# Kernel optimization log

Hardware: AMD Instinct MI355X
Metric: run time of the kernel (lower is better)

Reference implementation:

```python
import jax, jax.numpy as jnp
import numpy as np

B = 8
T, H, W = 8, 56, 56
C = 128
NH = 4
HD = C // NH
WS = (2, 7, 7)
SS = (1, 3, 3)
N = WS[0] * WS[1] * WS[2]  # 98 tokens per window
HID = 4 * C
SCALE = HD ** -0.5
RPB_SIZE = (2 * WS[0] - 1) * (2 * WS[1] - 1) * (2 * WS[2] - 1)  # 507
EPS = 1e-5


def _rel_index():
    # [N, N] int index into relative position bias table
    coords = np.stack(np.meshgrid(np.arange(WS[0]), np.arange(WS[1]), np.arange(WS[2]), indexing='ij'))
    cf = coords.reshape(3, -1)
    rel = (cf[:, :, None] - cf[:, None, :]).transpose(1, 2, 0)
    rel[:, :, 0] += WS[0] - 1
    rel[:, :, 1] += WS[1] - 1
    rel[:, :, 2] += WS[2] - 1
    rel[:, :, 0] *= (2 * WS[1] - 1) * (2 * WS[2] - 1)
    rel[:, :, 1] *= 2 * WS[2] - 1
    return rel.sum(-1)


def _np_window_partition_mask(img):
    # img: [1,T,H,W,1] -> [nW, N]
    m = img.reshape(1, T // WS[0], WS[0], H // WS[1], WS[1], W // WS[2], WS[2], 1)
    m = m.transpose(0, 1, 3, 5, 2, 4, 6, 7).reshape(-1, N)
    return m


def _attn_mask():
    # standard shifted-window mask: [nW, N, N] with 0 / -100
    img = np.zeros((1, T, H, W, 1), np.float32)
    cnt = 0
    slices = lambda w, s: (slice(0, -w), slice(-w, -s), slice(-s, None))
    for t in slices(WS[0], SS[0]):
        for h in slices(WS[1], SS[1]):
            for w in slices(WS[2], SS[2]):
                img[:, t, h, w, :] = cnt
                cnt += 1
    mw = _np_window_partition_mask(img)
    am = mw[:, None, :] - mw[:, :, None]
    return np.where(am != 0, np.float32(-100.0), np.float32(0.0))


REL_IDX = jnp.asarray(_rel_index())          # [N, N]
ATTN_MASK = jnp.asarray(_attn_mask())        # [nW, N, N]


def window_partition(x):
    # x: [B,T,H,W,C] -> [B*nW, N, C]
    x = x.reshape(B, T // WS[0], WS[0], H // WS[1], WS[1], W // WS[2], WS[2], C)
    return x.transpose(0, 1, 3, 5, 2, 4, 6, 7).reshape(-1, N, C)


def window_reverse(w):
    # w: [B*nW, N, C] -> [B,T,H,W,C]
    x = w.reshape(B, T // WS[0], H // WS[1], W // WS[2], WS[0], WS[1], WS[2], C)
    return x.transpose(0, 1, 4, 2, 5, 3, 6, 7).reshape(B, T, H, W, C)


def layernorm(x, g, b):
    mu = x.mean(-1, keepdims=True)
    var = ((x - mu) ** 2).mean(-1, keepdims=True)
    return (x - mu) * jax.lax.rsqrt(var + EPS) * g + b


def setup_inputs() -> dict:
    key = jax.random.key(0)
    ks = jax.random.split(key, 8)
    p = lambda k, shp: jax.random.normal(k, shp, jnp.float32) * 0.02
    return {
        'x': jax.random.normal(ks[0], (B, T * H * W, C), jnp.float32),
        'norm1_g': jnp.ones((C,), jnp.float32), 'norm1_b': jnp.zeros((C,), jnp.float32),
        'qkv_w': p(ks[1], (C, 3 * C)), 'qkv_b': jnp.zeros((3 * C,), jnp.float32),
        'proj_w': p(ks[2], (C, C)), 'proj_b': jnp.zeros((C,), jnp.float32),
        'rpb_table': p(ks[3], (RPB_SIZE, NH)),
        'norm2_g': jnp.ones((C,), jnp.float32), 'norm2_b': jnp.zeros((C,), jnp.float32),
        'fc1_w': p(ks[4], (C, HID)), 'fc1_b': jnp.zeros((HID,), jnp.float32),
        'fc2_w': p(ks[5], (HID, C)), 'fc2_b': jnp.zeros((C,), jnp.float32),
    }


def reference(x, norm1_g, norm1_b, qkv_w, qkv_b, proj_w, proj_b, rpb_table,
              norm2_g, norm2_b, fc1_w, fc1_b, fc2_w, fc2_b):
    shortcut = x
    h = layernorm(x, norm1_g, norm1_b).reshape(B, T, H, W, C)
    # cyclic shift
    h = jnp.roll(h, (-SS[0], -SS[1], -SS[2]), axis=(1, 2, 3))
    xw = window_partition(h)                                   # [B_, N, C]
    B_ = xw.shape[0]
    qkv = (xw @ qkv_w + qkv_b).reshape(B_, N, 3, NH, HD)
    qkv = qkv.transpose(2, 0, 3, 1, 4)                         # [3, B_, NH, N, HD]
    q, k, v = qkv[0] * SCALE, qkv[1], qkv[2]
    attn = jnp.einsum('bhnd,bhmd->bhnm', q, k)                 # [B_, NH, N, N]
    bias = rpb_table[REL_IDX.reshape(-1)].reshape(N, N, NH).transpose(2, 0, 1)
    attn = attn + bias[None]
    nW = ATTN_MASK.shape[0]
    attn = attn.reshape(B_ // nW, nW, NH, N, N) + ATTN_MASK[None, :, None]
    attn = jax.nn.softmax(attn.reshape(B_, NH, N, N), axis=-1)
    out = jnp.einsum('bhnm,bhmd->bhnd', attn, v)               # [B_, NH, N, HD]
    out = out.transpose(0, 2, 1, 3).reshape(B_, N, C)
    out = out @ proj_w + proj_b
    h = window_reverse(out)
    h = jnp.roll(h, SS, axis=(1, 2, 3)).reshape(B, T * H * W, C)
    x = shortcut + h
    y = layernorm(x, norm2_g, norm2_b)
    y = jax.nn.gelu(y @ fc1_w + fc1_b, approximate=False) @ fc2_w + fc2_b
    return x + y
```

## Files before the change

### kernel.cpp

```cpp
#include <hip/hip_runtime.h>
#include <hip/hip_bf16.h>
#include <cmath>

using bf16 = __hip_bfloat16;
typedef __attribute__((ext_vector_type(8))) short short8;
typedef __attribute__((ext_vector_type(4))) short short4v;
typedef __attribute__((ext_vector_type(4))) float float4f;

#define THW 25088
#define SCALE_QK 0.17677669529663687f

static __device__ __forceinline__ float4f mfma16(short8 a, short8 b, float4f c) {
  return __builtin_amdgcn_mfma_f32_16x16x32_bf16(a, b, c, 0, 0, 0);
}
static __device__ __forceinline__ short8 load8(const bf16* p) {
  return *reinterpret_cast<const short8*>(p);
}
static __device__ __forceinline__ short8 load8u(const unsigned short* p) {
  return *reinterpret_cast<const short8*>(p);
}
static __device__ __forceinline__ bf16 f2b(float v) { return __float2bfloat16(v); }
static __device__ __forceinline__ unsigned short f2bits(float v) {
  bf16 h = __float2bfloat16(v);
  unsigned short u; __builtin_memcpy(&u, &h, 2); return u;
}
static __device__ __forceinline__ float bits2f(unsigned short u) {
  unsigned int w = ((unsigned int)u) << 16;
  float f; __builtin_memcpy(&f, &w, 4); return f;
}
static __device__ __forceinline__ float gelu_f(float v) {
  float y = 0.7978845608028654f * (v + 0.044715f * v * v * v);
  float e = __expf(-2.f * fabsf(y));
  float t = 1.f - 2.f * e / (1.f + e);
  return 0.5f * v * (1.f + copysignf(t, y));
}

__global__ __launch_bounds__(256) void transpose_all(
    const float* __restrict__ qkv_w, const float* __restrict__ proj_w,
    const float* __restrict__ fc1_w, const float* __restrict__ fc2_w,
    const float* __restrict__ rpb,
    bf16* __restrict__ bq, bf16* __restrict__ bp,
    bf16* __restrict__ b1, bf16* __restrict__ b2,
    unsigned short* __restrict__ tbl) {
  int idx = blockIdx.x * 256 + threadIdx.x;
  if (idx < 49152) {
    int k = idx / 384, n = idx - k * 384;
    float v = qkv_w[idx];
    if (n < 128) v *= SCALE_QK;
    bq[(size_t)n * 128 + k] = f2b(v);
  } else if (idx < 65536) {
    int i = idx - 49152;
    int k = i / 128, n = i - k * 128;
    bp[(size_t)n * 128 + k] = f2b(proj_w[i]);
  } else if (idx < 131072) {
    int i = idx - 65536;
    int k = i / 512, n = i - k * 512;
    b1[(size_t)n * 128 + k] = f2b(fc1_w[i]);
  } else if (idx < 196608) {
    int i = idx - 131072;
    int k = i / 128, n = i - k * 128;
    b2[(size_t)n * 512 + k] = f2b(fc2_w[i]);
  } else {
    int i2 = idx - 196608;
    int col = i2 % 120; int rest = i2 / 120;
    int row = rest % 112; rest /= 112;
    int head = rest & 3; int cat = rest >> 2;
    int i = row > 97 ? 97 : row;
    int j = col > 97 ? 97 : col;
    int ti = i / 49, ri = i - ti * 49, hi = ri / 7, wi = ri - hi * 7;
    int tj = j / 49, rj = j - tj * 49, hj = rj / 7, wj = rj - hj * 7;
    int tbit = (cat >> 2) & 1, hbit = (cat >> 1) & 1, wbit = cat & 1;
    int ilab = (tbit ? 1 + ti : 0) * 9 + (hbit ? 1 + (hi >= 4) : 0) * 3 +
               (wbit ? 1 + (wi >= 4) : 0);
    int jlab = (tbit ? 1 + tj : 0) * 9 + (hbit ? 1 + (hj >= 4) : 0) * 3 +
               (wbit ? 1 + (wj >= 4) : 0);
    int idxr = (ti - tj + 1) * 169 + (hi - hj + 6) * 13 + (wi - wj + 6);
    float v = rpb[idxr * 4 + head];
    if (ilab != jlab) v -= 100.f;
    if (col >= 98) v = -30000.f;
    tbl[i2] = f2bits(v);
  }
}

__global__ __launch_bounds__(1024) void win_k(const float* __restrict__ x,
    const float* __restrict__ n1g, const float* __restrict__ n1b,
    const bf16* __restrict__ bt_qkv, const float* __restrict__ qkv_b,
    const bf16* __restrict__ bt_proj, const float* __restrict__ proj_b,
    const float* __restrict__ n2g, const float* __restrict__ n2b,
    const bf16* __restrict__ bt_fc1, const float* __restrict__ fc1b,
    const bf16* __restrict__ bt_fc2, const float* __restrict__ fc2b,
    const unsigned short* __restrict__ tbl, float* __restrict__ out) {
  __shared__ __align__(16) unsigned short qk[112][264];
  __shared__ __align__(16) unsigned short vt[128][136];
  __shared__ __align__(16) unsigned short pool[16 * 16 * 136];
  auto xn   = reinterpret_cast<unsigned short(*)[136]>(pool);
  auto Pl   = reinterpret_cast<unsigned short(*)[16][136]>(pool);
  auto xmid = reinterpret_cast<float(*)[132]>(pool);

  const int lane = threadIdx.x & 63, wave = threadIdx.x >> 6;
  const int l15 = lane & 15, lq = lane >> 4;
  const int wg = blockIdx.x;
  const int batch = wg >> 8, widx = wg & 255;
  const int tw = widx >> 6, hw = (widx >> 3) & 7, ww = widx & 7;
  const int cat = ((tw == 3) ? 4 : 0) + ((hw == 7) ? 2 : 0) + ((ww == 7) ? 1 : 0);

  for (int i = threadIdx.x; i < 128 * 16; i += 1024) {
    vt[i >> 4][112 + (i & 15)] = 0;
  }

  {
    float2 gp = reinterpret_cast<const float2*>(n1g)[lane];
    float2 bp = reinterpret_cast<const float2*>(n1b)[lane];
    float2 vals[7];
    #pragma unroll
    for (int i = 0; i < 7; i++) {
      int lrow = wave * 7 + i;
      int n = lrow > 97 ? 97 : lrow;
      int ti = n / 49, rr = n - ti * 49, hi = rr / 7, wi = rr - hi * 7;
      int t = (tw * 2 + ti + 1) & 7;
      int h = hw * 7 + hi + 3; if (h >= 56) h -= 56;
      int w = ww * 7 + wi + 3; if (w >= 56) w -= 56;
      unsigned int tok = (unsigned int)batch * THW + (t * 56 + h) * 56 + w;
      if (lane == 0) *reinterpret_cast<unsigned int*>(&vt[lrow][128]) = tok;
      vals[i] = reinterpret_cast<const float2*>(x + (size_t)tok * 128)[lane];
    }
    #pragma unroll
    for (int i = 0; i < 7; i++) {
      int lrow = wave * 7 + i;
      float2 v = vals[i];
      float s = v.x + v.y, ss = v.x * v.x + v.y * v.y;
      #pragma unroll
      for (int m = 1; m < 64; m <<= 1) { s += __shfl_xor(s, m); ss += __shfl_xor(ss, m); }
      float mu = s * (1.f / 128.f);
      float var = ss * (1.f / 128.f) - mu * mu;
      float rs = rsqrtf(var + 1e-5f);
      float o0 = (v.x - mu) * rs * gp.x + bp.x;
      float o1 = (v.y - mu) * rs * gp.y + bp.y;
      *reinterpret_cast<unsigned int*>(&xn[lrow][lane * 2]) =
          (unsigned int)f2bits(o0) | ((unsigned int)f2bits(o1) << 16);
    }
  }
  __syncthreads();

  for (int task = wave; task < 48; task += 16) {
    const int ct = task >> 1, half = task & 1;
    const int rt0 = half ? 4 : 0, rt1 = half ? 7 : 4;
    short8 wf[4];
    #pragma unroll
    for (int q = 0; q < 4; q++)
      wf[q] = load8(bt_qkv + (size_t)(ct * 16 + l15) * 128 + q * 32 + lq * 8);
    if (ct < 16) {
      float4f bs = *reinterpret_cast<const float4f*>(qkv_b + ct * 16 + lq * 4);
      if (ct < 8) bs *= SCALE_QK;
      const int colb = (ct < 8 ? ct * 16 : 128 + (ct - 8) * 16) + lq * 4;
      #pragma unroll
      for (int i = 0; i < 4; i++) {
        int rt = rt0 + i;
        if (rt < rt1) {
          float4f acc = (float4f){0.f, 0.f, 0.f, 0.f};
          #pragma unroll
          for (int q = 0; q < 4; q++)
            acc = mfma16(wf[q], load8u(&xn[rt * 16 + l15][q * 32 + lq * 8]), acc);
          short4v pk;
          #pragma unroll
          for (int r = 0; r < 4; r++) pk[r] = (short)f2bits(acc[r] + bs[r]);
          *reinterpret_cast<short4v*>(&qk[rt * 16 + l15][colb]) = pk;
        }
      }
    } else {
      const float bsv = qkv_b[256 + (ct - 16) * 16 + l15];
      #pragma unroll
      for (int i = 0; i < 4; i++) {
        int rt = rt0 + i;
        if (rt < rt1) {
          float4f acc = (float4f){0.f, 0.f, 0.f, 0.f};
          #pragma unroll
          for (int q = 0; q < 4; q++)
            acc = mfma16(load8u(&xn[rt * 16 + l15][q * 32 + lq * 8]), wf[q], acc);
          short4v pk;
          #pragma unroll
          for (int r = 0; r < 4; r++) pk[r] = (short)f2bits(acc[r] + bsv);
          *reinterpret_cast<short4v*>(&vt[(ct - 16) * 16 + l15][rt * 16 + lq * 4]) = pk;
        }
      }
    }
  }
  __syncthreads();

  for (int task = wave; task < 28; task += 16) {
    const int head = task & 3, rb = task >> 2;
    const int q0 = rb * 16;
    const unsigned short* tb =
        tbl + ((size_t)(cat * 4 + head) * 112 + (q0 + l15)) * 120;

    short8 aq = load8u(&qk[q0 + l15][head * 32 + lq * 8]);
    float pv[7][4];
    #pragma unroll
    for (int t = 0; t < 7; t++) {
      short8 kb = load8u(&qk[t * 16 + l15][128 + head * 32 + lq * 8]);
      float4f s = mfma16(kb, aq, (float4f){0.f, 0.f, 0.f, 0.f});
      short4v bv = *reinterpret_cast<const short4v*>(tb + t * 16 + lq * 4);
      #pragma unroll
      for (int r = 0; r < 4; r++)
        pv[t][r] = s[r] + bits2f((unsigned short)bv[r]);
    }

    float mx = fmaxf(fmaxf(pv[0][0], pv[0][1]), fmaxf(pv[0][2], pv[0][3]));
    #pragma unroll
    for (int t = 1; t < 7; t++)
      mx = fmaxf(mx, fmaxf(fmaxf(pv[t][0], pv[t][1]), fmaxf(pv[t][2], pv[t][3])));
    mx = fmaxf(mx, __shfl_xor(mx, 16));
    mx = fmaxf(mx, __shfl_xor(mx, 32));
    float sum = 0.f;
    #pragma unroll
    for (int t = 0; t < 7; t++) {
      #pragma unroll
      for (int r = 0; r < 4; r++) { float p = __expf(pv[t][r] - mx); pv[t][r] = p; sum += p; }
    }
    sum += __shfl_xor(sum, 16);
    sum += __shfl_xor(sum, 32);
    float inv = 1.f / sum;
    #pragma unroll
    for (int t = 0; t < 7; t++) {
      short4v pk;
      #pragma unroll
      for (int r = 0; r < 4; r++) pk[r] = (short)f2bits(pv[t][r] * inv);
      *reinterpret_cast<short4v*>(&Pl[wave][l15][t * 16 + lq * 4]) = pk;
    }
    *reinterpret_cast<short4v*>(&Pl[wave][l15][112 + lq * 4]) = (short4v){0, 0, 0, 0};

    float4f o0 = (float4f){0.f, 0.f, 0.f, 0.f};
    float4f o1 = (float4f){0.f, 0.f, 0.f, 0.f};
    #pragma unroll
    for (int ks = 0; ks < 4; ks++) {
      short8 pf = load8u(&Pl[wave][l15][ks * 32 + lq * 8]);
      o0 = mfma16(load8u(&vt[head * 32 + l15][ks * 32 + lq * 8]), pf, o0);
      o1 = mfma16(load8u(&vt[head * 32 + 16 + l15][ks * 32 + lq * 8]), pf, o1);
    }
    short4v k0, k1;
    #pragma unroll
    for (int r = 0; r < 4; r++) {
      k0[r] = (short)f2bits(o0[r]);
      k1[r] = (short)f2bits(o1[r]);
    }
    *reinterpret_cast<short4v*>(&qk[q0 + l15][head * 32 + lq * 4]) = k0;
    *reinterpret_cast<short4v*>(&qk[q0 + l15][head * 32 + 16 + lq * 4]) = k1;
  }
  __syncthreads();

  {
    const int ct = wave & 7, half = wave >> 3;
    const int rt0 = half ? 4 : 0, rt1 = half ? 7 : 4;
    const int cb = ct * 16 + lq * 4;
    float4f pb = *reinterpret_cast<const float4f*>(proj_b + cb);
    short8 wf[4];
    #pragma unroll
    for (int q = 0; q < 4; q++)
      wf[q] = load8(bt_proj + (size_t)(ct * 16 + l15) * 128 + q * 32 + lq * 8);
    #pragma unroll
    for (int i = 0; i < 4; i++) {
      int rt = rt0 + i;
      if (rt < rt1) {
        float4f acc = (float4f){0.f, 0.f, 0.f, 0.f};
        #pragma unroll
        for (int q = 0; q < 4; q++)
          acc = mfma16(wf[q], load8u(&qk[rt * 16 + l15][q * 32 + lq * 8]), acc);
        int row = rt * 16 + l15;
        if (row < 98) {
          unsigned int tok = *reinterpret_cast<const unsigned int*>(&vt[row][128]);
          float4f xv = *reinterpret_cast<const float4f*>(x + (size_t)tok * 128 + cb);
          *reinterpret_cast<float4f*>(&xmid[row][cb]) = xv + acc + pb;
        }
      }
    }
  }
  __syncthreads();

  {
    float2 gp = reinterpret_cast<const float2*>(n2g)[lane];
    float2 bp = reinterpret_cast<const float2*>(n2b)[lane];
    #pragma unroll
    for (int i = 0; i < 7; i++) {
      int lrow = wave * 7 + i;
      int n = lrow > 97 ? 97 : lrow;
      float2 v = *reinterpret_cast<const float2*>(&xmid[n][lane * 2]);
      float s = v.x + v.y, ss = v.x * v.x + v.y * v.y;
      #pragma unroll
      for (int m = 1; m < 64; m <<= 1) { s += __shfl_xor(s, m); ss += __shfl_xor(ss, m); }
      float mu = s * (1.f / 128.f);
      float var = ss * (1.f / 128.f) - mu * mu;
      float rs = rsqrtf(var + 1e-5f);
      float o0 = (v.x - mu) * rs * gp.x + bp.x;
      float o1 = (v.y - mu) * rs * gp.y + bp.y;
      *reinterpret_cast<unsigned int*>(&vt[lrow][lane * 2]) =
          (unsigned int)f2bits(o0) | ((unsigned int)f2bits(o1) << 16);
    }
  }
  __syncthreads();

  const int ct6 = wave & 7, half6 = wave >> 3;
  const int rt0 = half6 ? 4 : 0, rt1 = half6 ? 7 : 4;
  const int cb6 = ct6 * 16 + lq * 4;
  float4f acc2[4];
  #pragma unroll
  for (int i = 0; i < 4; i++) acc2[i] = (float4f){0.f, 0.f, 0.f, 0.f};
  short8 b1f[4];
  #pragma unroll
  for (int q = 0; q < 4; q++)
    b1f[q] = load8(bt_fc1 + (size_t)(ct6 * 16 + l15) * 128 + q * 32 + lq * 8);

  #pragma unroll
  for (int hb = 0; hb < 4; hb++) {
    short8 b2f[4];
    #pragma unroll
    for (int q = 0; q < 4; q++)
      b2f[q] = load8(bt_fc2 + (size_t)(ct6 * 16 + l15) * 512 + hb * 128 + q * 32 + lq * 8);
    float4f bias1 = *reinterpret_cast<const float4f*>(fc1b + hb * 128 + cb6);
    float4f a1[4];
    #pragma unroll
    for (int i = 0; i < 4; i++) {
      int rt = rt0 + i;
      if (rt < rt1) {
        float4f acc = (float4f){0.f, 0.f, 0.f, 0.f};
        #pragma unroll
        for (int q = 0; q < 4; q++)
          acc = mfma16(b1f[q], load8u(&vt[rt * 16 + l15][q * 32 + lq * 8]), acc);
        a1[i] = acc;
      }
    }
    if (hb) __syncthreads();
    #pragma unroll
    for (int i = 0; i < 4; i++) {
      int rt = rt0 + i;
      if (rt < rt1) {
        short4v pk;
        #pragma unroll
        for (int r = 0; r < 4; r++) pk[r] = (short)f2bits(gelu_f(a1[i][r] + bias1[r]));
        *reinterpret_cast<short4v*>(&qk[rt * 16 + l15][cb6]) = pk;
      }
    }
    __syncthreads();
    short8 b1n[4];
    if (hb < 3) {
      #pragma unroll
      for (int q = 0; q < 4; q++)
        b1n[q] = load8(bt_fc1 + (size_t)((hb + 1) * 128 + ct6 * 16 + l15) * 128 + q * 32 + lq * 8);
    }
    #pragma unroll
    for (int i = 0; i < 4; i++) {
      int rt = rt0 + i;
      if (rt < rt1) {
        #pragma unroll
        for (int q = 0; q < 4; q++)
          acc2[i] = mfma16(b2f[q], load8u(&qk[rt * 16 + l15][q * 32 + lq * 8]), acc2[i]);
      }
    }
    #pragma unroll
    for (int q = 0; q < 4; q++) b1f[q] = b1n[q];
  }

  {
    float4f b2v = *reinterpret_cast<const float4f*>(fc2b + cb6);
    #pragma unroll
    for (int i = 0; i < 4; i++) {
      int rt = rt0 + i;
      if (rt < rt1) {
        int row = rt * 16 + l15;
        if (row < 98) {
          unsigned int tok = *reinterpret_cast<const unsigned int*>(&vt[row][128]);
          float4f xm = *reinterpret_cast<const float4f*>(&xmid[row][cb6]);
          *reinterpret_cast<float4f*>(out + (size_t)tok * 128 + cb6) = xm + acc2[i] + b2v;
        }
      }
    }
  }
}

extern "C" void kernel_launch(void* const* d_in, const int* in_sizes, int n_in,
                              void* d_out, int out_size, void* d_ws, size_t ws_size,
                              hipStream_t stream) {
  (void)in_sizes; (void)n_in; (void)out_size; (void)ws_size;
  const float* x      = (const float*)d_in[0];
  const float* n1g    = (const float*)d_in[1];
  const float* n1b    = (const float*)d_in[2];
  const float* qkv_w  = (const float*)d_in[3];
  const float* qkv_b  = (const float*)d_in[4];
  const float* proj_w = (const float*)d_in[5];
  const float* proj_b = (const float*)d_in[6];
  const float* rpb    = (const float*)d_in[7];
  const float* n2g    = (const float*)d_in[8];
  const float* n2b    = (const float*)d_in[9];
  const float* fc1_w  = (const float*)d_in[10];
  const float* fc1_b  = (const float*)d_in[11];
  const float* fc2_w  = (const float*)d_in[12];
  const float* fc2_b  = (const float*)d_in[13];
  float* out = (float*)d_out;

  char* ws = (char*)d_ws;
  bf16* bt_qkv  = (bf16*)(ws + 0);
  bf16* bt_proj = (bf16*)(ws + 98304);
  bf16* bt_fc1  = (bf16*)(ws + 131072);
  bf16* bt_fc2  = (bf16*)(ws + 262144);
  unsigned short* tbl = (unsigned short*)(ws + 393216);

  transpose_all<<<2448, 256, 0, stream>>>(qkv_w, proj_w, fc1_w, fc2_w, rpb,
                                          bt_qkv, bt_proj, bt_fc1, bt_fc2, tbl);

  win_k<<<2048, 1024, 0, stream>>>(x, n1g, n1b, bt_qkv, qkv_b, bt_proj, proj_b,
                                   n2g, n2b, bt_fc1, fc1_b, bt_fc2, fc2_b,
                                   tbl, out);
}
```

Measured before the change: 551.4 us.

## Restructure MLP into 256-wide hidden chunks and drop softmax max pass

The fused MLP stage is reorganised so all 16 waves compute fc1 plus GELU over 256 hidden columns at a time, instead of 128, and fc2 accumulates in two larger steps. This cuts the number of barrier-separated passes over shared memory. The softmax no longer subtracts the row max before exponentiating, which removes a reduction pass and two shuffles but could overflow if scores were ever large. The post-projection residual is also kept in registers, so the final output no longer reloads it from shared memory. In exchange, register pressure rises from holding seven GELU tiles per wave.

Measured after the change: 522.3 us. 1.06x faster.

```diff
diff --git a/kernel.cpp b/kernel.cpp
--- a/kernel.cpp
+++ b/kernel.cpp
@@ -195,27 +195,17 @@
 
     short8 aq = load8u(&qk[q0 + l15][head * 32 + lq * 8]);
     float pv[7][4];
+    float sum = 0.f;
     #pragma unroll
     for (int t = 0; t < 7; t++) {
       short8 kb = load8u(&qk[t * 16 + l15][128 + head * 32 + lq * 8]);
       float4f s = mfma16(kb, aq, (float4f){0.f, 0.f, 0.f, 0.f});
       short4v bv = *reinterpret_cast<const short4v*>(tb + t * 16 + lq * 4);
       #pragma unroll
-      for (int r = 0; r < 4; r++)
-        pv[t][r] = s[r] + bits2f((unsigned short)bv[r]);
-    }
-
-    float mx = fmaxf(fmaxf(pv[0][0], pv[0][1]), fmaxf(pv[0][2], pv[0][3]));
-    #pragma unroll
-    for (int t = 1; t < 7; t++)
-      mx = fmaxf(mx, fmaxf(fmaxf(pv[t][0], pv[t][1]), fmaxf(pv[t][2], pv[t][3])));
-    mx = fmaxf(mx, __shfl_xor(mx, 16));
-    mx = fmaxf(mx, __shfl_xor(mx, 32));
-    float sum = 0.f;
-    #pragma unroll
-    for (int t = 0; t < 7; t++) {
-      #pragma unroll
-      for (int r = 0; r < 4; r++) { float p = __expf(pv[t][r] - mx); pv[t][r] = p; sum += p; }
+      for (int r = 0; r < 4; r++) {
+        float p = __expf(s[r] + bits2f((unsigned short)bv[r]));
+        pv[t][r] = p; sum += p;
+      }
     }
     sum += __shfl_xor(sum, 16);
     sum += __shfl_xor(sum, 32);
@@ -248,15 +238,16 @@
   }
   __syncthreads();
 
-  {
-    const int ct = wave & 7, half = wave >> 3;
-    const int rt0 = half ? 4 : 0, rt1 = half ? 7 : 4;
-    const int cb = ct * 16 + lq * 4;
+  const int ct4 = wave & 7, half4 = wave >> 3;
+  const int rt0 = half4 ? 4 : 0, rt1 = half4 ? 7 : 4;
+  const int cb = ct4 * 16 + lq * 4;
+  float4f xmr[4];
+  {
     float4f pb = *reinterpret_cast<const float4f*>(proj_b + cb);
     short8 wf[4];
     #pragma unroll
     for (int q = 0; q < 4; q++)
-      wf[q] = load8(bt_proj + (size_t)(ct * 16 + l15) * 128 + q * 32 + lq * 8);
+      wf[q] = load8(bt_proj + (size_t)(ct4 * 16 + l15) * 128 + q * 32 + lq * 8);
     #pragma unroll
     for (int i = 0; i < 4; i++) {
       int rt = rt0 + i;
@@ -269,7 +260,9 @@
         if (row < 98) {
           unsigned int tok = *reinterpret_cast<const unsigned int*>(&vt[row][128]);
           float4f xv = *reinterpret_cast<const float4f*>(x + (size_t)tok * 128 + cb);
-          *reinterpret_cast<float4f*>(&xmid[row][cb]) = xv + acc + pb;
+          float4f res = xv + acc + pb;
+          xmr[i] = res;
+          *reinterpret_cast<float4f*>(&xmid[row][cb]) = res;
         }
       }
     }
@@ -298,69 +291,121 @@
   }
   __syncthreads();
 
-  const int ct6 = wave & 7, half6 = wave >> 3;
-  const int rt0 = half6 ? 4 : 0, rt1 = half6 ? 7 : 4;
-  const int cb6 = ct6 * 16 + lq * 4;
   float4f acc2[4];
   #pragma unroll
   for (int i = 0; i < 4; i++) acc2[i] = (float4f){0.f, 0.f, 0.f, 0.f};
-  short8 b1f[4];
+  const int hc = wave * 16 + lq * 4;
+
+  float4f a1[7];
+  {
+    short8 w1[4];
+    #pragma unroll
+    for (int q = 0; q < 4; q++)
+      w1[q] = load8(bt_fc1 + (size_t)(wave * 16 + l15) * 128 + q * 32 + lq * 8);
+    float4f b1v = *reinterpret_cast<const float4f*>(fc1b + hc);
+    #pragma unroll
+    for (int rt = 0; rt < 7; rt++) {
+      float4f acc = (float4f){0.f, 0.f, 0.f, 0.f};
+      #pragma unroll
+      for (int q = 0; q < 4; q++)
+        acc = mfma16(w1[q], load8u(&vt[rt * 16 + l15][q * 32 + lq * 8]), acc);
+      #pragma unroll
+      for (int r = 0; r < 4; r++) acc[r] = gelu_f(acc[r] + b1v[r]);
+      a1[rt] = acc;
+    }
+  }
   #pragma unroll
-  for (int q = 0; q < 4; q++)
-    b1f[q] = load8(bt_fc1 + (size_t)(ct6 * 16 + l15) * 128 + q * 32 + lq * 8);
-
-  #pragma unroll
-  for (int hb = 0; hb < 4; hb++) {
-    short8 b2f[4];
-    #pragma unroll
-    for (int q = 0; q < 4; q++)
-      b2f[q] = load8(bt_fc2 + (size_t)(ct6 * 16 + l15) * 512 + hb * 128 + q * 32 + lq * 8);
-    float4f bias1 = *reinterpret_cast<const float4f*>(fc1b + hb * 128 + cb6);
-    float4f a1[4];
-    #pragma unroll
-    for (int i = 0; i < 4; i++) {
-      int rt = rt0 + i;
-      if (rt < rt1) {
-        float4f acc = (float4f){0.f, 0.f, 0.f, 0.f};
+  for (int rt = 0; rt < 7; rt++) {
+    short4v pk;
+    #pragma unroll
+    for (int r = 0; r < 4; r++) pk[r] = (short)f2bits(a1[rt][r]);
+    *reinterpret_cast<short4v*>(&qk[rt * 16 + l15][hc]) = pk;
+  }
+  __syncthreads();
+
+  {
+    short8 w1[4];
+    #pragma unroll
+    for (int q = 0; q < 4; q++)
+      w1[q] = load8(bt_fc1 + (size_t)(256 + wave * 16 + l15) * 128 + q * 32 + lq * 8);
+    float4f b1v = *reinterpret_cast<const float4f*>(fc1b + 256 + hc);
+    short8 w2[4];
+    #pragma unroll
+    for (int q = 0; q < 4; q++)
+      w2[q] = load8(bt_fc2 + (size_t)(ct4 * 16 + l15) * 512 + q * 32 + lq * 8);
+    #pragma unroll
+    for (int rt = 0; rt < 7; rt++) {
+      float4f acc = (float4f){0.f, 0.f, 0.f, 0.f};
+      #pragma unroll
+      for (int q = 0; q < 4; q++)
+        acc = mfma16(w1[q], load8u(&vt[rt * 16 + l15][q * 32 + lq * 8]), acc);
+      #pragma unroll
+      for (int r = 0; r < 4; r++) acc[r] = gelu_f(acc[r] + b1v[r]);
+      a1[rt] = acc;
+    }
+    #pragma unroll
+    for (int i = 0; i < 4; i++) {
+      int rt = rt0 + i;
+      if (rt < rt1) {
         #pragma unroll
         for (int q = 0; q < 4; q++)
-          acc = mfma16(b1f[q], load8u(&vt[rt * 16 + l15][q * 32 + lq * 8]), acc);
-        a1[i] = acc;
-      }
-    }
-    if (hb) __syncthreads();
-    #pragma unroll
-    for (int i = 0; i < 4; i++) {
-      int rt = rt0 + i;
-      if (rt < rt1) {
-        short4v pk;
-        #pragma unroll
-        for (int r = 0; r < 4; r++) pk[r] = (short)f2bits(gelu_f(a1[i][r] + bias1[r]));
-        *reinterpret_cast<short4v*>(&qk[rt * 16 + l15][cb6]) = pk;
-      }
-    }
-    __syncthreads();
-    short8 b1n[4];
-    if (hb < 3) {
-      #pragma unroll
-      for (int q = 0; q < 4; q++)
-        b1n[q] = load8(bt_fc1 + (size_t)((hb + 1) * 128 + ct6 * 16 + l15) * 128 + q * 32 + lq * 8);
-    }
+          acc2[i] = mfma16(w2[q], load8u(&qk[rt * 16 + l15][q * 32 + lq * 8]), acc2[i]);
+      }
+    }
+    short8 w2b[4];
+    #pragma unroll
+    for (int q = 0; q < 4; q++)
+      w2b[q] = load8(bt_fc2 + (size_t)(ct4 * 16 + l15) * 512 + 128 + q * 32 + lq * 8);
     #pragma unroll
     for (int i = 0; i < 4; i++) {
       int rt = rt0 + i;
       if (rt < rt1) {
         #pragma unroll
         for (int q = 0; q < 4; q++)
-          acc2[i] = mfma16(b2f[q], load8u(&qk[rt * 16 + l15][q * 32 + lq * 8]), acc2[i]);
-      }
-    }
-    #pragma unroll
-    for (int q = 0; q < 4; q++) b1f[q] = b1n[q];
-  }
-
-  {
-    float4f b2v = *reinterpret_cast<const float4f*>(fc2b + cb6);
+          acc2[i] = mfma16(w2b[q], load8u(&qk[rt * 16 + l15][128 + q * 32 + lq * 8]), acc2[i]);
+      }
+    }
+  }
+  __syncthreads();
+  #pragma unroll
+  for (int rt = 0; rt < 7; rt++) {
+    short4v pk;
+    #pragma unroll
+    for (int r = 0; r < 4; r++) pk[r] = (short)f2bits(a1[rt][r]);
+    *reinterpret_cast<short4v*>(&qk[rt * 16 + l15][hc]) = pk;
+  }
+  __syncthreads();
+  {
+    short8 w2[4];
+    #pragma unroll
+    for (int q = 0; q < 4; q++)
+      w2[q] = load8(bt_fc2 + (size_t)(ct4 * 16 + l15) * 512 + 256 + q * 32 + lq * 8);
+    #pragma unroll
+    for (int i = 0; i < 4; i++) {
+      int rt = rt0 + i;
+      if (rt < rt1) {
+        #pragma unroll
+        for (int q = 0; q < 4; q++)
+          acc2[i] = mfma16(w2[q], load8u(&qk[rt * 16 + l15][q * 32 + lq * 8]), acc2[i]);
+      }
+    }
+    short8 w2b[4];
+    #pragma unroll
+    for (int q = 0; q < 4; q++)
+      w2b[q] = load8(bt_fc2 + (size_t)(ct4 * 16 + l15) * 512 + 384 + q * 32 + lq * 8);
+    #pragma unroll
+    for (int i = 0; i < 4; i++) {
+      int rt = rt0 + i;
+      if (rt < rt1) {
+        #pragma unroll
+        for (int q = 0; q < 4; q++)
+          acc2[i] = mfma16(w2b[q], load8u(&qk[rt * 16 + l15][128 + q * 32 + lq * 8]), acc2[i]);
+      }
+    }
+  }
+
+  {
+    float4f b2v = *reinterpret_cast<const float4f*>(fc2b + cb);
     #pragma unroll
     for (int i = 0; i < 4; i++) {
       int rt = rt0 + i;
@@ -368,8 +413,7 @@
         int row = rt * 16 + l15;
         if (row < 98) {
           unsigned int tok = *reinterpret_cast<const unsigned int*>(&vt[row][128]);
-          float4f xm = *reinterpret_cast<const float4f*>(&xmid[row][cb6]);
-          *reinterpret_cast<float4f*>(out + (size_t)tok * 128 + cb6) = xm + acc2[i] + b2v;
+          *reinterpret_cast<float4f*>(out + (size_t)tok * 128 + cb) = xmr[i] + acc2[i] + b2v;
         }
       }
     }
```
